# Kernel tuning notes

Hardware: AMD Instinct MI355X
Metric: run time of the kernel (lower is better)

The kernel has to match this reference:

```python
import jax, jax.numpy as jnp
import numpy as np

B, L, D, H = 2, 2048, 1024, 16
DH = D // H
EPS = 1e-5


def setup_inputs() -> dict:
    key = jax.random.key(0)
    ks = jax.random.split(key, 8)
    s = 0.02  # realistic init scale for weights
    # causal mask: True where attention is DISALLOWED (masked_fill semantics)
    mask = jnp.triu(jnp.ones((L, L), dtype=bool), k=1)[None, None]  # [1,1,L,L]
    return {
        "x": jax.random.normal(ks[0], (B, L, D), jnp.float32),
        "mask": mask,
        "ln_g": jnp.ones((D,), jnp.float32),
        "ln_b": jnp.zeros((D,), jnp.float32),
        "Wq": jax.random.normal(ks[1], (D, D), jnp.float32) * s,
        "bq": jnp.zeros((D,), jnp.float32),
        "Wk": jax.random.normal(ks[2], (D, D), jnp.float32) * s,
        "bk": jnp.zeros((D,), jnp.float32),
        "Wv": jax.random.normal(ks[3], (D, D), jnp.float32) * s,
        "bv": jnp.zeros((D,), jnp.float32),
        "Wo": jax.random.normal(ks[4], (D, D), jnp.float32) * s,
        "bo": jnp.zeros((D,), jnp.float32),
    }


def _layernorm(x, g, b):
    mu = jnp.mean(x, axis=-1, keepdims=True)
    var = jnp.var(x, axis=-1, keepdims=True)
    return (x - mu) * jax.lax.rsqrt(var + EPS) * g + b


def reference(x, mask, ln_g, ln_b, Wq, bq, Wk, bk, Wv, bv, Wo, bo):
    b, l, d = x.shape
    h = _layernorm(x, ln_g, ln_b)
    # separate Q/K/V linears, split into heads: [b, H, l, DH]
    q = (h @ Wq + bq).reshape(b, l, H, DH).transpose(0, 2, 1, 3)
    k = (h @ Wk + bk).reshape(b, l, H, DH).transpose(0, 2, 1, 3)
    v = (h @ Wv + bv).reshape(b, l, H, DH).transpose(0, 2, 1, 3)
    scale = jnp.asarray(DH, x.dtype) ** -0.5
    # full L x L score matrix (this is exactly what the torch module does)
    w = jnp.einsum("bhqd,bhkd->bhqk", q, k) * scale
    w = jnp.where(mask, -jnp.inf, w)
    w = jax.nn.softmax(w, axis=-1)
    # dropout layers are identity in eval mode
    o = jnp.einsum("bhqk,bhkd->bhqd", w, v)
    o = o.transpose(0, 2, 1, 3).reshape(b, l, d)
    return o @ Wo + bo
```

## Files before the change

### kernel.cpp

```cpp
#include <hip/hip_runtime.h>
#include <hip/hip_bf16.h>


typedef __bf16  bf16x8 __attribute__((ext_vector_type(8)));
typedef __bf16  bf16x4 __attribute__((ext_vector_type(4)));
typedef float   f32x4  __attribute__((ext_vector_type(4)));
typedef float   f32x16 __attribute__((ext_vector_type(16)));
typedef unsigned int u32x2 __attribute__((ext_vector_type(2)));
typedef unsigned int u32x4 __attribute__((ext_vector_type(4)));

#define MFMA16(a, b, c) __builtin_amdgcn_mfma_f32_16x16x32_bf16(a, b, c, 0, 0, 0)
#define MFMA32(a, b, c) __builtin_amdgcn_mfma_f32_32x32x16_bf16(a, b, c, 0, 0, 0)

#define LDT 72
#define LDO 68

#define QSCALE 0.18033688011112042f

__device__ __forceinline__ void gl_lds16(const void* g, void* l) {
    __builtin_amdgcn_global_load_lds(
        (const __attribute__((address_space(1))) void*)g,
        (__attribute__((address_space(3))) void*)l, 16, 0, 0);
}

__global__ __launch_bounds__(256) void ln_kernel(
    const float* __restrict__ x, const float* __restrict__ g,
    const float* __restrict__ bta, __hip_bfloat16* __restrict__ h)
{
    __shared__ float red[8];
    const int row = blockIdx.x, t = threadIdx.x;
    const float* xr = x + (size_t)row * 1024;
    const float4 xv = *(const float4*)(xr + t * 4);
    float s  = xv.x + xv.y + xv.z + xv.w;
    float ss = xv.x * xv.x + xv.y * xv.y + xv.z * xv.z + xv.w * xv.w;
    #pragma unroll
    for (int off = 32; off > 0; off >>= 1) {
        s  += __shfl_down(s, off);
        ss += __shfl_down(ss, off);
    }
    const int lane = t & 63, wave = t >> 6;
    if (lane == 0) { red[wave] = s; red[4 + wave] = ss; }
    __syncthreads();
    const float S  = red[0] + red[1] + red[2] + red[3];
    const float SS = red[4] + red[5] + red[6] + red[7];
    const float mu   = S * (1.0f / 1024.0f);
    const float var  = SS * (1.0f / 1024.0f) - mu * mu;
    const float rstd = rsqrtf(var + 1e-5f);
    const float4 gv = *(const float4*)(g + t * 4);
    const float4 bv = *(const float4*)(bta + t * 4);
    bf16x4 hv;
    hv[0] = (__bf16)((xv.x - mu) * rstd * gv.x + bv.x);
    hv[1] = (__bf16)((xv.y - mu) * rstd * gv.y + bv.y);
    hv[2] = (__bf16)((xv.z - mu) * rstd * gv.z + bv.z);
    hv[3] = (__bf16)((xv.w - mu) * rstd * gv.w + bv.w);
    *(bf16x4*)(h + (size_t)row * 1024 + t * 4) = hv;
}

__global__ void transpose_cast_kernel(
    const float* __restrict__ Wq, const float* __restrict__ Wk,
    const float* __restrict__ Wv, const float* __restrict__ Wo,
    __hip_bfloat16* __restrict__ tq, __hip_bfloat16* __restrict__ tk,
    __hip_bfloat16* __restrict__ tv, __hip_bfloat16* __restrict__ to_)
{
    __shared__ float t[32][33];
    const int z = blockIdx.z;
    const float* src = (z == 0) ? Wq : (z == 1) ? Wk : (z == 2) ? Wv : Wo;
    __hip_bfloat16* dst = (z == 0) ? tq : (z == 1) ? tk : (z == 2) ? tv : to_;
    const int n0 = blockIdx.x * 32, k0 = blockIdx.y * 32;
    const int tx = threadIdx.x, ty = threadIdx.y;
    t[ty][tx] = src[(size_t)(k0 + ty) * 1024 + n0 + tx];
    __syncthreads();
    dst[(size_t)(n0 + ty) * 1024 + k0 + tx] = __float2bfloat16(t[tx][ty]);
}

__device__ __forceinline__ void gemm_core_1024(
    const __hip_bfloat16* __restrict__ A, const __hip_bfloat16* __restrict__ Bt,
    int m0, int n0, f32x4 (&acc)[4][2])
{
    __shared__ __align__(16) __hip_bfloat16 sA[128 * 64];
    __shared__ __align__(16) __hip_bfloat16 sB[128 * 64];
    const int tid  = threadIdx.x;
    const int wave = tid >> 6, lane = tid & 63;
    const int quad = lane >> 4, l16 = lane & 15;
    const int wm = wave >> 2, wn = wave & 3;

    const f32x4 zero = {0.f, 0.f, 0.f, 0.f};
    #pragma unroll
    for (int i = 0; i < 4; ++i)
        #pragma unroll
        for (int j = 0; j < 2; ++j) acc[i][j] = zero;

    const int r0 = tid >> 3;
    const int c0 = (((tid & 7) ^ (r0 & 7)) << 3);
    const __hip_bfloat16* Ap = A  + (size_t)(m0 + r0) * 1024 + c0;
    const __hip_bfloat16* Bp = Bt + (size_t)(n0 + r0) * 1024 + c0;
    __hip_bfloat16* lA0 = sA + tid * 8;
    __hip_bfloat16* lB0 = sB + tid * 8;

    const int rsw = l16 & 7;

    for (int k0 = 0; k0 < 1024; k0 += 64) {
        __syncthreads();
        gl_lds16(Ap + k0, lA0);
        gl_lds16(Ap + (size_t)64 * 1024 + k0, lA0 + 64 * 64);
        gl_lds16(Bp + k0, lB0);
        gl_lds16(Bp + (size_t)64 * 1024 + k0, lB0 + 64 * 64);
        __syncthreads();
        #pragma unroll
        for (int kk = 0; kk < 64; kk += 32) {
            const int sl = (((quad + (kk >> 3)) ^ rsw) << 3);
            bf16x8 af[4], bfr[2];
            #pragma unroll
            for (int mt = 0; mt < 4; ++mt)
                af[mt] = *(const bf16x8*)(sA + (wm * 64 + mt * 16 + l16) * 64 + sl);
            #pragma unroll
            for (int nt = 0; nt < 2; ++nt)
                bfr[nt] = *(const bf16x8*)(sB + (wn * 32 + nt * 16 + l16) * 64 + sl);
            #pragma unroll
            for (int mt = 0; mt < 4; ++mt)
                #pragma unroll
                for (int nt = 0; nt < 2; ++nt)
                    acc[mt][nt] = MFMA16(af[mt], bfr[nt], acc[mt][nt]);
        }
    }
}

__global__ __launch_bounds__(512) void gemm_qkv_kernel(
    const __hip_bfloat16* __restrict__ h,
    const __hip_bfloat16* __restrict__ wt_base,
    const float* __restrict__ bq, const float* __restrict__ bk,
    const float* __restrict__ bv,
    __hip_bfloat16* __restrict__ qkv_base)
{
    const int z = blockIdx.z;
    const __hip_bfloat16* wt = wt_base + ((size_t)z << 20);
    __hip_bfloat16* outp = qkv_base + ((size_t)z << 22);

    const bool swp = (z == 2);
    const __hip_bfloat16* A  = swp ? wt : h;
    const __hip_bfloat16* Bt = swp ? h  : wt;
    const int m0 = swp ? blockIdx.x * 128 : blockIdx.y * 128;
    const int n0 = swp ? blockIdx.y * 128 : blockIdx.x * 128;

    f32x4 acc[4][2];
    gemm_core_1024(A, Bt, m0, n0, acc);

    const int lane = threadIdx.x & 63, wave = threadIdx.x >> 6;
    const int quad = lane >> 4, l16 = lane & 15;
    const int wm = wave >> 2, wn = wave & 3;

    if (!swp) {
        const float* bias = (z == 0) ? bq : bk;
        const float scale = (z == 0) ? QSCALE : 1.0f;
        #pragma unroll
        for (int mt = 0; mt < 4; ++mt)
            #pragma unroll
            for (int nt = 0; nt < 2; ++nt)
                #pragma unroll
                for (int r = 0; r < 4; ++r) {
                    const int gm = m0 + wm * 64 + mt * 16 + quad * 4 + r;
                    const int gn = n0 + wn * 32 + nt * 16 + l16;
                    const float v = (acc[mt][nt][r] + bias[gn]) * scale;
                    const int b = gm >> 11, l = gm & 2047;
                    const int hh = gn >> 6, dh = gn & 63;
                    outp[(((((size_t)(b * 16 + hh)) << 11) + l) * 64) + dh] = __float2bfloat16(v);
                }
    } else {
        #pragma unroll
        for (int mt = 0; mt < 4; ++mt)
            #pragma unroll
            for (int nt = 0; nt < 2; ++nt)
                #pragma unroll
                for (int r = 0; r < 4; ++r) {
                    const int rr = m0 + wm * 64 + mt * 16 + quad * 4 + r;
                    const int cc = n0 + wn * 32 + nt * 16 + l16;
                    const float v = acc[mt][nt][r] + bv[rr];
                    const int b = cc >> 11, l = cc & 2047;
                    const int hh = rr >> 6, dh = rr & 63;
                    outp[((((size_t)(b * 16 + hh)) * 64 + dh) << 11) + l] = __float2bfloat16(v);
                }
    }
}

__global__ __launch_bounds__(512) void gemm_out_kernel(
    const __hip_bfloat16* __restrict__ o, const __hip_bfloat16* __restrict__ wot,
    const float* __restrict__ bo, float* __restrict__ out)
{
    __shared__ __align__(16) __hip_bfloat16 sA[64 * 64];
    __shared__ __align__(16) __hip_bfloat16 sB[128 * 64];
    const int tid  = threadIdx.x;
    const int wave = tid >> 6, lane = tid & 63;
    const int quad = lane >> 4, l16 = lane & 15;
    const int wm = wave >> 2, wn = wave & 3;
    const int m0 = blockIdx.y * 64, n0 = blockIdx.x * 128;

    const f32x4 zero = {0.f, 0.f, 0.f, 0.f};
    f32x4 acc[2][2];
    #pragma unroll
    for (int i = 0; i < 2; ++i)
        #pragma unroll
        for (int j = 0; j < 2; ++j) acc[i][j] = zero;

    const int r0 = tid >> 3;
    const int c0 = (((tid & 7) ^ (r0 & 7)) << 3);
    const __hip_bfloat16* Ap = o   + (size_t)(m0 + r0) * 1024 + c0;
    const __hip_bfloat16* Bp = wot + (size_t)(n0 + r0) * 1024 + c0;
    __hip_bfloat16* lA0 = sA + tid * 8;
    __hip_bfloat16* lB0 = sB + tid * 8;

    const int rsw = l16 & 7;

    for (int k0 = 0; k0 < 1024; k0 += 64) {
        __syncthreads();
        gl_lds16(Ap + k0, lA0);
        gl_lds16(Bp + k0, lB0);
        gl_lds16(Bp + (size_t)64 * 1024 + k0, lB0 + 64 * 64);
        __syncthreads();
        #pragma unroll
        for (int kk = 0; kk < 64; kk += 32) {
            const int sl = (((quad + (kk >> 3)) ^ rsw) << 3);
            bf16x8 af[2], bfr[2];
            #pragma unroll
            for (int mt = 0; mt < 2; ++mt)
                af[mt] = *(const bf16x8*)(sA + (wm * 32 + mt * 16 + l16) * 64 + sl);
            #pragma unroll
            for (int nt = 0; nt < 2; ++nt)
                bfr[nt] = *(const bf16x8*)(sB + (wn * 32 + nt * 16 + l16) * 64 + sl);
            #pragma unroll
            for (int mt = 0; mt < 2; ++mt)
                #pragma unroll
                for (int nt = 0; nt < 2; ++nt)
                    acc[mt][nt] = MFMA16(af[mt], bfr[nt], acc[mt][nt]);
        }
    }

    #pragma unroll
    for (int mt = 0; mt < 2; ++mt)
        #pragma unroll
        for (int nt = 0; nt < 2; ++nt)
            #pragma unroll
            for (int r = 0; r < 4; ++r) {
                const int gm = m0 + wm * 32 + mt * 16 + quad * 4 + r;
                const int gn = n0 + wn * 32 + nt * 16 + l16;
                out[(size_t)gm * 1024 + gn] = acc[mt][nt][r] + bo[gn];
            }
}

__global__ __launch_bounds__(512, 4) void attn_kernel(
    const __hip_bfloat16* __restrict__ Q,
    const __hip_bfloat16* __restrict__ Kg,
    const __hip_bfloat16* __restrict__ Vt,
    __hip_bfloat16* __restrict__ O)
{
    __shared__ __align__(16) char smem[36864];
    __hip_bfloat16* sK = (__hip_bfloat16*)smem;
    __hip_bfloat16* sV = (__hip_bfloat16*)(smem + 18432);

    const int tid  = threadIdx.x;
    const int wave = tid >> 6, lane = tid & 63;
    const int grp  = wave >> 2, w4 = wave & 3;
    const int wk = w4 >> 1, wq = w4 & 1;
    const int q5 = lane & 31, hi = lane >> 5;
    const int bh = blockIdx.x;
    const int qt = 31 - blockIdx.y;
    const int q0 = qt * 64;

    const __hip_bfloat16* Qp = Q  + (size_t)bh * 2048 * 64;
    const __hip_bfloat16* Kp = Kg + (size_t)bh * 2048 * 64;
    const __hip_bfloat16* Vp = Vt + (size_t)bh * 64 * 2048;

    bf16x8 Qf[4];
    #pragma unroll
    for (int ks = 0; ks < 4; ++ks)
        Qf[ks] = *(const bf16x8*)(Qp + (size_t)(q0 + wq * 32 + q5) * 64 + ks * 16 + hi * 8);

    f32x16 o0, o1;
    #pragma unroll
    for (int r = 0; r < 16; ++r) { o0[r] = 0.f; o1[r] = 0.f; }
    float l_run = 0.f;

    const __hip_bfloat16* sKg = sK + grp * (64 * LDT);
    const __hip_bfloat16* sVg = sV + grp * (64 * LDT);
    const int qloc = wq * 32 + q5;

    const int sg = tid >> 8, tt = tid & 255;
    __hip_bfloat16* dK = sK + sg * (64 * LDT);
    __hip_bfloat16* dV = sV + sg * (64 * LDT);

    const int R = (qt + 2) >> 1;

    for (int r = 0; r < R; ++r) {
        __syncthreads();
        const int js = 2 * r + sg;
        if (js <= qt) {
            const int k0 = js * 64;
            #pragma unroll
            for (int i = 0; i < 2; ++i) {
                const int chunk = tt + 256 * i, rr = chunk >> 3, cc = (chunk & 7) << 3;
                *(int4*)(dK + rr * LDT + cc) = *(const int4*)(Kp + (size_t)(k0 + rr) * 64 + cc);
                *(int4*)(dV + rr * LDT + cc) = *(const int4*)(Vp + (size_t)rr * 2048 + k0 + cc);
            }
        }
        __syncthreads();

        const int j = 2 * r + grp;
        if (j <= qt) {
            const bool diag = (j == qt);
            f32x16 s;
            #pragma unroll
            for (int i = 0; i < 16; ++i) s[i] = 0.f;
            __builtin_amdgcn_s_setprio(1);
            #pragma unroll
            for (int ks = 0; ks < 4; ++ks) {
                const bf16x8 kf = *(const bf16x8*)(sKg + (wk * 32 + q5) * LDT + ks * 16 + hi * 8);
                s = MFMA32(kf, Qf[ks], s);
            }
            __builtin_amdgcn_s_setprio(0);
            if (diag) {
                #pragma unroll
                for (int i = 0; i < 16; ++i) {
                    const int krow = wk * 32 + (i & 3) + 8 * (i >> 2) + 4 * hi;
                    if (krow > qloc) s[i] = -1e30f;
                }
            }
            float rs = 0.f;
            u32x2 U[4];
            #pragma unroll
            for (int rb = 0; rb < 4; ++rb) {
                bf16x4 pk;
                #pragma unroll
                for (int c = 0; c < 4; ++c) {
                    const float p = exp2f(s[rb * 4 + c]);
                    rs += p;
                    pk[c] = (__bf16)p;
                }
                U[rb] = __builtin_bit_cast(u32x2, pk);
            }
            rs += __shfl_xor(rs, 32);
            l_run += rs;
            __builtin_amdgcn_s_setprio(1);
            #pragma unroll
            for (int t = 0; t < 2; ++t) {
                const unsigned p0a = __shfl_xor(U[2 * t][0], 32);
                const unsigned p0b = __shfl_xor(U[2 * t][1], 32);
                const unsigned p1a = __shfl_xor(U[2 * t + 1][0], 32);
                const unsigned p1b = __shfl_xor(U[2 * t + 1][1], 32);
                const unsigned w0 = hi ? p1a : U[2 * t][0];
                const unsigned w1 = hi ? p1b : U[2 * t][1];
                const unsigned w2 = hi ? U[2 * t + 1][0] : p0a;
                const unsigned w3 = hi ? U[2 * t + 1][1] : p0b;
                const u32x4 pw = {w0, w1, w2, w3};
                const bf16x8 pf = __builtin_bit_cast(bf16x8, pw);
                const bf16x8 vf0 = *(const bf16x8*)(sVg + (q5)      * LDT + wk * 32 + 16 * t + 8 * hi);
                const bf16x8 vf1 = *(const bf16x8*)(sVg + (32 + q5) * LDT + wk * 32 + 16 * t + 8 * hi);
                o0 = MFMA32(vf0, pf, o0);
                o1 = MFMA32(vf1, pf, o1);
            }
            __builtin_amdgcn_s_setprio(0);
        }
    }

    __syncthreads();
    float* Oscr = (float*)smem;
    float* lscr = (float*)(smem + 17408);

    if (hi == 0)
        lscr[(grp * 2 + wk) * 64 + wq * 32 + q5] = l_run;

    auto wrO = [&](bool add) {
        float* rowp = Oscr + (wq * 32 + q5) * LDO;
        #pragma unroll
        for (int d = 0; d < 2; ++d) {
            const f32x16& oc = d ? o1 : o0;
            #pragma unroll
            for (int rb = 0; rb < 4; ++rb) {
                float* p = rowp + d * 32 + 8 * rb + 4 * hi;
                f32x4 v;
                if (add) {
                    v = *(const f32x4*)p;
                    v[0] += oc[rb * 4 + 0]; v[1] += oc[rb * 4 + 1];
                    v[2] += oc[rb * 4 + 2]; v[3] += oc[rb * 4 + 3];
                } else {
                    v[0] = oc[rb * 4 + 0]; v[1] = oc[rb * 4 + 1];
                    v[2] = oc[rb * 4 + 2]; v[3] = oc[rb * 4 + 3];
                }
                *(f32x4*)p = v;
            }
        }
    };
    if (grp == 1 && wk == 1) wrO(false);
    __syncthreads();
    if (grp == 1 && wk == 0) wrO(true);
    __syncthreads();
    if (grp == 0 && wk == 1) wrO(true);
    __syncthreads();
    if (grp == 0 && wk == 0) wrO(true);
    __syncthreads();

    const int b = bh >> 4, hh = bh & 15;
    const int row = tid >> 3, col = (tid & 7) << 3;
    const float lt = lscr[(0 * 2 + 0) * 64 + row] + lscr[(0 * 2 + 1) * 64 + row]
                   + lscr[(1 * 2 + 0) * 64 + row] + lscr[(1 * 2 + 1) * 64 + row];
    const float linv = 1.0f / lt;
    const float* src = Oscr + row * LDO + col;
    const f32x4 v0 = *(const f32x4*)src;
    const f32x4 v1 = *(const f32x4*)(src + 4);
    bf16x8 ov;
    ov[0] = (__bf16)(v0[0] * linv); ov[1] = (__bf16)(v0[1] * linv);
    ov[2] = (__bf16)(v0[2] * linv); ov[3] = (__bf16)(v0[3] * linv);
    ov[4] = (__bf16)(v1[0] * linv); ov[5] = (__bf16)(v1[1] * linv);
    ov[6] = (__bf16)(v1[2] * linv); ov[7] = (__bf16)(v1[3] * linv);
    *(bf16x8*)(O + ((size_t)b * 2048 + q0 + row) * 1024 + hh * 64 + col) = ov;
}

extern "C" void kernel_launch(void* const* d_in, const int* in_sizes, int n_in,
                              void* d_out, int out_size, void* d_ws, size_t ws_size,
                              hipStream_t stream) {
    const float* x    = (const float*)d_in[0];
    const float* ln_g = (const float*)d_in[2];
    const float* ln_b = (const float*)d_in[3];
    const float* Wq = (const float*)d_in[4];  const float* bq = (const float*)d_in[5];
    const float* Wk = (const float*)d_in[6];  const float* bk = (const float*)d_in[7];
    const float* Wv = (const float*)d_in[8];  const float* bv = (const float*)d_in[9];
    const float* Wo = (const float*)d_in[10]; const float* bo = (const float*)d_in[11];
    float* out = (float*)d_out;

    __hip_bfloat16* ws = (__hip_bfloat16*)d_ws;
    const size_t M1 = 1024 * 1024;
    __hip_bfloat16* h   = ws;
    __hip_bfloat16* wqt = ws + 4 * M1;
    __hip_bfloat16* wot = ws + 7 * M1;
    __hip_bfloat16* q   = ws + 8 * M1;
    __hip_bfloat16* k   = ws + 12 * M1;
    __hip_bfloat16* vt  = ws + 16 * M1;
    __hip_bfloat16* o   = h;

    ln_kernel<<<4096, 256, 0, stream>>>(x, ln_g, ln_b, h);
    transpose_cast_kernel<<<dim3(32, 32, 4), dim3(32, 32), 0, stream>>>(
        Wq, Wk, Wv, Wo, wqt, wqt + M1, wqt + 2 * M1, wot);
    gemm_qkv_kernel<<<dim3(8, 32, 3), 512, 0, stream>>>(h, wqt, bq, bk, bv, q);
    attn_kernel<<<dim3(32, 32), 512, 0, stream>>>(q, k, vt, o);
    gemm_out_kernel<<<dim3(8, 64), 512, 0, stream>>>(o, wot, bo, out);
}
```

Before: 198.5 us.

## Double-buffer attention K/V tiles via async global_load_lds with XOR-swizzled LDS

```diff
diff --git a/kernel.cpp b/kernel.cpp
--- a/kernel.cpp
+++ b/kernel.cpp
@@ -12,7 +12,6 @@
 #define MFMA16(a, b, c) __builtin_amdgcn_mfma_f32_16x16x32_bf16(a, b, c, 0, 0, 0)
 #define MFMA32(a, b, c) __builtin_amdgcn_mfma_f32_32x32x16_bf16(a, b, c, 0, 0, 0)
 
-#define LDT 72
 #define LDO 68
 
 #define QSCALE 0.18033688011112042f
@@ -252,9 +251,9 @@
     const __hip_bfloat16* __restrict__ Vt,
     __hip_bfloat16* __restrict__ O)
 {
-    __shared__ __align__(16) char smem[36864];
+    __shared__ __align__(16) char smem[65536];
     __hip_bfloat16* sK = (__hip_bfloat16*)smem;
-    __hip_bfloat16* sV = (__hip_bfloat16*)(smem + 18432);
+    __hip_bfloat16* sV = (__hip_bfloat16*)(smem + 32768);
 
     const int tid  = threadIdx.x;
     const int wave = tid >> 6, lane = tid & 63;
@@ -279,40 +278,49 @@
     for (int r = 0; r < 16; ++r) { o0[r] = 0.f; o1[r] = 0.f; }
     float l_run = 0.f;
 
-    const __hip_bfloat16* sKg = sK + grp * (64 * LDT);
-    const __hip_bfloat16* sVg = sV + grp * (64 * LDT);
     const int qloc = wq * 32 + q5;
-
-    const int sg = tid >> 8, tt = tid & 255;
-    __hip_bfloat16* dK = sK + sg * (64 * LDT);
-    __hip_bfloat16* dV = sV + sg * (64 * LDT);
+    const int rxor = q5 & 7;
+
+    const int srow = tid >> 3;
+    const int scol = (((tid & 7) ^ (srow & 7)) << 3);
+    const __hip_bfloat16* Kst = Kp + (size_t)srow * 64 + scol;
+    const __hip_bfloat16* Vst = Vp + (size_t)srow * 2048 + scol;
+    __hip_bfloat16* dK = sK + tid * 8;
+    __hip_bfloat16* dV = sV + tid * 8;
+
+    auto stage = [&](int g, int j, int p) {
+        const int k0 = j * 64;
+        const int off = ((p * 2 + g) << 12);
+        gl_lds16(Kst + (size_t)k0 * 64, dK + off);
+        gl_lds16(Vst + k0,              dV + off);
+    };
+
+    stage(0, 0, 0);
+    if (qt >= 1) stage(1, 1, 0);
+    __syncthreads();
 
     const int R = (qt + 2) >> 1;
 
     for (int r = 0; r < R; ++r) {
-        __syncthreads();
-        const int js = 2 * r + sg;
-        if (js <= qt) {
-            const int k0 = js * 64;
-            #pragma unroll
-            for (int i = 0; i < 2; ++i) {
-                const int chunk = tt + 256 * i, rr = chunk >> 3, cc = (chunk & 7) << 3;
-                *(int4*)(dK + rr * LDT + cc) = *(const int4*)(Kp + (size_t)(k0 + rr) * 64 + cc);
-                *(int4*)(dV + rr * LDT + cc) = *(const int4*)(Vp + (size_t)rr * 2048 + k0 + cc);
-            }
+        const int p = r & 1;
+        const int jn = 2 * r + 2;
+        if (jn <= qt) {
+            stage(0, jn, p ^ 1);
+            if (jn + 1 <= qt) stage(1, jn + 1, p ^ 1);
         }
-        __syncthreads();
-
         const int j = 2 * r + grp;
         if (j <= qt) {
             const bool diag = (j == qt);
+            const __hip_bfloat16* sKg = sK + ((p * 2 + grp) << 12);
+            const __hip_bfloat16* sVg = sV + ((p * 2 + grp) << 12);
             f32x16 s;
             #pragma unroll
             for (int i = 0; i < 16; ++i) s[i] = 0.f;
             __builtin_amdgcn_s_setprio(1);
             #pragma unroll
             for (int ks = 0; ks < 4; ++ks) {
-                const bf16x8 kf = *(const bf16x8*)(sKg + (wk * 32 + q5) * LDT + ks * 16 + hi * 8);
+                const bf16x8 kf = *(const bf16x8*)(
+                    sKg + (wk * 32 + q5) * 64 + (((ks * 2 + hi) ^ rxor) << 3));
                 s = MFMA32(kf, Qf[ks], s);
             }
             __builtin_amdgcn_s_setprio(0);
@@ -330,9 +338,9 @@
                 bf16x4 pk;
                 #pragma unroll
                 for (int c = 0; c < 4; ++c) {
-                    const float p = exp2f(s[rb * 4 + c]);
-                    rs += p;
-                    pk[c] = (__bf16)p;
+                    const float p2 = exp2f(s[rb * 4 + c]);
+                    rs += p2;
+                    pk[c] = (__bf16)p2;
                 }
                 U[rb] = __builtin_bit_cast(u32x2, pk);
             }
@@ -351,16 +359,17 @@
                 const unsigned w3 = hi ? U[2 * t + 1][1] : p0b;
                 const u32x4 pw = {w0, w1, w2, w3};
                 const bf16x8 pf = __builtin_bit_cast(bf16x8, pw);
-                const bf16x8 vf0 = *(const bf16x8*)(sVg + (q5)      * LDT + wk * 32 + 16 * t + 8 * hi);
-                const bf16x8 vf1 = *(const bf16x8*)(sVg + (32 + q5) * LDT + wk * 32 + 16 * t + 8 * hi);
+                const int sl = ((wk * 4 + 2 * t + hi) ^ rxor) << 3;
+                const bf16x8 vf0 = *(const bf16x8*)(sVg + (q5)      * 64 + sl);
+                const bf16x8 vf1 = *(const bf16x8*)(sVg + (32 + q5) * 64 + sl);
                 o0 = MFMA32(vf0, pf, o0);
                 o1 = MFMA32(vf1, pf, o1);
             }
             __builtin_amdgcn_s_setprio(0);
         }
+        __syncthreads();
     }
 
-    __syncthreads();
     float* Oscr = (float*)smem;
     float* lscr = (float*)(smem + 17408);
 
```

Result: no change. 199.2 us (+0.3%).

## Shrink attention block to 4 waves with double-buffered K/V tiles

Applied to the files above, without the earlier changes.

```diff
diff --git a/kernel.cpp b/kernel.cpp
--- a/kernel.cpp
+++ b/kernel.cpp
@@ -246,7 +246,7 @@
             }
 }
 
-__global__ __launch_bounds__(512, 4) void attn_kernel(
+__global__ __launch_bounds__(256, 4) void attn_kernel(
     const __hip_bfloat16* __restrict__ Q,
     const __hip_bfloat16* __restrict__ Kg,
     const __hip_bfloat16* __restrict__ Vt,
@@ -258,8 +258,7 @@
 
     const int tid  = threadIdx.x;
     const int wave = tid >> 6, lane = tid & 63;
-    const int grp  = wave >> 2, w4 = wave & 3;
-    const int wk = w4 >> 1, wq = w4 & 1;
+    const int wk = wave >> 1, wq = wave & 1;
     const int q5 = lane & 31, hi = lane >> 5;
     const int bh = blockIdx.x;
     const int qt = 31 - blockIdx.y;
@@ -279,85 +278,81 @@
     for (int r = 0; r < 16; ++r) { o0[r] = 0.f; o1[r] = 0.f; }
     float l_run = 0.f;
 
-    const __hip_bfloat16* sKg = sK + grp * (64 * LDT);
-    const __hip_bfloat16* sVg = sV + grp * (64 * LDT);
     const int qloc = wq * 32 + q5;
 
-    const int sg = tid >> 8, tt = tid & 255;
-    __hip_bfloat16* dK = sK + sg * (64 * LDT);
-    __hip_bfloat16* dV = sV + sg * (64 * LDT);
-
-    const int R = (qt + 2) >> 1;
-
-    for (int r = 0; r < R; ++r) {
+    auto stage = [&](int j, int buf) {
+        const int k0 = j * 64;
+        __hip_bfloat16* dK = sK + buf * (64 * LDT);
+        __hip_bfloat16* dV = sV + buf * (64 * LDT);
+        #pragma unroll
+        for (int i = 0; i < 2; ++i) {
+            const int chunk = tid + 256 * i, rr = chunk >> 3, cc = (chunk & 7) << 3;
+            *(int4*)(dK + rr * LDT + cc) = *(const int4*)(Kp + (size_t)(k0 + rr) * 64 + cc);
+            *(int4*)(dV + rr * LDT + cc) = *(const int4*)(Vp + (size_t)rr * 2048 + k0 + cc);
+        }
+    };
+
+    stage(0, 0);
+
+    for (int j = 0; j <= qt; ++j) {
+        const int cur = j & 1;
         __syncthreads();
-        const int js = 2 * r + sg;
-        if (js <= qt) {
-            const int k0 = js * 64;
-            #pragma unroll
-            for (int i = 0; i < 2; ++i) {
-                const int chunk = tt + 256 * i, rr = chunk >> 3, cc = (chunk & 7) << 3;
-                *(int4*)(dK + rr * LDT + cc) = *(const int4*)(Kp + (size_t)(k0 + rr) * 64 + cc);
-                *(int4*)(dV + rr * LDT + cc) = *(const int4*)(Vp + (size_t)rr * 2048 + k0 + cc);
+        if (j < qt) stage(j + 1, cur ^ 1);
+
+        const __hip_bfloat16* sKg = sK + cur * (64 * LDT);
+        const __hip_bfloat16* sVg = sV + cur * (64 * LDT);
+        const bool diag = (j == qt);
+        f32x16 s;
+        #pragma unroll
+        for (int i = 0; i < 16; ++i) s[i] = 0.f;
+        __builtin_amdgcn_s_setprio(1);
+        #pragma unroll
+        for (int ks = 0; ks < 4; ++ks) {
+            const bf16x8 kf = *(const bf16x8*)(sKg + (wk * 32 + q5) * LDT + ks * 16 + hi * 8);
+            s = MFMA32(kf, Qf[ks], s);
+        }
+        __builtin_amdgcn_s_setprio(0);
+        if (diag) {
+            #pragma unroll
+            for (int i = 0; i < 16; ++i) {
+                const int krow = wk * 32 + (i & 3) + 8 * (i >> 2) + 4 * hi;
+                if (krow > qloc) s[i] = -1e30f;
             }
         }
-        __syncthreads();
-
-        const int j = 2 * r + grp;
-        if (j <= qt) {
-            const bool diag = (j == qt);
-            f32x16 s;
-            #pragma unroll
-            for (int i = 0; i < 16; ++i) s[i] = 0.f;
-            __builtin_amdgcn_s_setprio(1);
-            #pragma unroll
-            for (int ks = 0; ks < 4; ++ks) {
-                const bf16x8 kf = *(const bf16x8*)(sKg + (wk * 32 + q5) * LDT + ks * 16 + hi * 8);
-                s = MFMA32(kf, Qf[ks], s);
+        float rs = 0.f;
+        u32x2 U[4];
+        #pragma unroll
+        for (int rb = 0; rb < 4; ++rb) {
+            bf16x4 pk;
+            #pragma unroll
+            for (int c = 0; c < 4; ++c) {
+                const float p = exp2f(s[rb * 4 + c]);
+                rs += p;
+                pk[c] = (__bf16)p;
             }
-            __builtin_amdgcn_s_setprio(0);
-            if (diag) {
-                #pragma unroll
-                for (int i = 0; i < 16; ++i) {
-                    const int krow = wk * 32 + (i & 3) + 8 * (i >> 2) + 4 * hi;
-                    if (krow > qloc) s[i] = -1e30f;
-                }
-            }
-            float rs = 0.f;
-            u32x2 U[4];
-            #pragma unroll
-            for (int rb = 0; rb < 4; ++rb) {
-                bf16x4 pk;
-                #pragma unroll
-                for (int c = 0; c < 4; ++c) {
-                    const float p = exp2f(s[rb * 4 + c]);
-                    rs += p;
-                    pk[c] = (__bf16)p;
-                }
-                U[rb] = __builtin_bit_cast(u32x2, pk);
-            }
-            rs += __shfl_xor(rs, 32);
-            l_run += rs;
-            __builtin_amdgcn_s_setprio(1);
-            #pragma unroll
-            for (int t = 0; t < 2; ++t) {
-                const unsigned p0a = __shfl_xor(U[2 * t][0], 32);
-                const unsigned p0b = __shfl_xor(U[2 * t][1], 32);
-                const unsigned p1a = __shfl_xor(U[2 * t + 1][0], 32);
-                const unsigned p1b = __shfl_xor(U[2 * t + 1][1], 32);
-                const unsigned w0 = hi ? p1a : U[2 * t][0];
-                const unsigned w1 = hi ? p1b : U[2 * t][1];
-                const unsigned w2 = hi ? U[2 * t + 1][0] : p0a;
-                const unsigned w3 = hi ? U[2 * t + 1][1] : p0b;
-                const u32x4 pw = {w0, w1, w2, w3};
-                const bf16x8 pf = __builtin_bit_cast(bf16x8, pw);
-                const bf16x8 vf0 = *(const bf16x8*)(sVg + (q5)      * LDT + wk * 32 + 16 * t + 8 * hi);
-                const bf16x8 vf1 = *(const bf16x8*)(sVg + (32 + q5) * LDT + wk * 32 + 16 * t + 8 * hi);
-                o0 = MFMA32(vf0, pf, o0);
-                o1 = MFMA32(vf1, pf, o1);
-            }
-            __builtin_amdgcn_s_setprio(0);
-        }
+            U[rb] = __builtin_bit_cast(u32x2, pk);
+        }
+        rs += __shfl_xor(rs, 32);
+        l_run += rs;
+        __builtin_amdgcn_s_setprio(1);
+        #pragma unroll
+        for (int t = 0; t < 2; ++t) {
+            const unsigned p0a = __shfl_xor(U[2 * t][0], 32);
+            const unsigned p0b = __shfl_xor(U[2 * t][1], 32);
+            const unsigned p1a = __shfl_xor(U[2 * t + 1][0], 32);
+            const unsigned p1b = __shfl_xor(U[2 * t + 1][1], 32);
+            const unsigned w0 = hi ? p1a : U[2 * t][0];
+            const unsigned w1 = hi ? p1b : U[2 * t][1];
+            const unsigned w2 = hi ? U[2 * t + 1][0] : p0a;
+            const unsigned w3 = hi ? U[2 * t + 1][1] : p0b;
+            const u32x4 pw = {w0, w1, w2, w3};
+            const bf16x8 pf = __builtin_bit_cast(bf16x8, pw);
+            const bf16x8 vf0 = *(const bf16x8*)(sVg + (q5)      * LDT + wk * 32 + 16 * t + 8 * hi);
+            const bf16x8 vf1 = *(const bf16x8*)(sVg + (32 + q5) * LDT + wk * 32 + 16 * t + 8 * hi);
+            o0 = MFMA32(vf0, pf, o0);
+            o1 = MFMA32(vf1, pf, o1);
+        }
+        __builtin_amdgcn_s_setprio(0);
     }
 
     __syncthreads();
@@ -365,7 +360,7 @@
     float* lscr = (float*)(smem + 17408);
 
     if (hi == 0)
-        lscr[(grp * 2 + wk) * 64 + wq * 32 + q5] = l_run;
+        lscr[wk * 64 + wq * 32 + q5] = l_run;
 
     auto wrO = [&](bool add) {
         float* rowp = Oscr + (wq * 32 + q5) * LDO;
@@ -388,29 +383,28 @@
             }
         }
     };
-    if (grp == 1 && wk == 1) wrO(false);
+    if (wk == 1) wrO(false);
     __syncthreads();
-    if (grp == 1 && wk == 0) wrO(true);
+    if (wk == 0) wrO(true);
     __syncthreads();
-    if (grp == 0 && wk == 1) wrO(true);
-    __syncthreads();
-    if (grp == 0 && wk == 0) wrO(true);
-    __syncthreads();
 
     const int b = bh >> 4, hh = bh & 15;
-    const int row = tid >> 3, col = (tid & 7) << 3;
-    const float lt = lscr[(0 * 2 + 0) * 64 + row] + lscr[(0 * 2 + 1) * 64 + row]
-                   + lscr[(1 * 2 + 0) * 64 + row] + lscr[(1 * 2 + 1) * 64 + row];
-    const float linv = 1.0f / lt;
-    const float* src = Oscr + row * LDO + col;
-    const f32x4 v0 = *(const f32x4*)src;
-    const f32x4 v1 = *(const f32x4*)(src + 4);
-    bf16x8 ov;
-    ov[0] = (__bf16)(v0[0] * linv); ov[1] = (__bf16)(v0[1] * linv);
-    ov[2] = (__bf16)(v0[2] * linv); ov[3] = (__bf16)(v0[3] * linv);
-    ov[4] = (__bf16)(v1[0] * linv); ov[5] = (__bf16)(v1[1] * linv);
-    ov[6] = (__bf16)(v1[2] * linv); ov[7] = (__bf16)(v1[3] * linv);
-    *(bf16x8*)(O + ((size_t)b * 2048 + q0 + row) * 1024 + hh * 64 + col) = ov;
+    #pragma unroll
+    for (int i = 0; i < 2; ++i) {
+        const int chunk = tid + 256 * i;
+        const int row = chunk >> 3, col = (chunk & 7) << 3;
+        const float lt = lscr[0 * 64 + row] + lscr[1 * 64 + row];
+        const float linv = 1.0f / lt;
+        const float* src = Oscr + row * LDO + col;
+        const f32x4 v0 = *(const f32x4*)src;
+        const f32x4 v1 = *(const f32x4*)(src + 4);
+        bf16x8 ov;
+        ov[0] = (__bf16)(v0[0] * linv); ov[1] = (__bf16)(v0[1] * linv);
+        ov[2] = (__bf16)(v0[2] * linv); ov[3] = (__bf16)(v0[3] * linv);
+        ov[4] = (__bf16)(v1[0] * linv); ov[5] = (__bf16)(v1[1] * linv);
+        ov[6] = (__bf16)(v1[2] * linv); ov[7] = (__bf16)(v1[3] * linv);
+        *(bf16x8*)(O + ((size_t)b * 2048 + q0 + row) * 1024 + hh * 64 + col) = ov;
+    }
 }
 
 extern "C" void kernel_launch(void* const* d_in, const int* in_sizes, int n_in,
@@ -439,6 +433,6 @@
     transpose_cast_kernel<<<dim3(32, 32, 4), dim3(32, 32), 0, stream>>>(
         Wq, Wk, Wv, Wo, wqt, wqt + M1, wqt + 2 * M1, wot);
     gemm_qkv_kernel<<<dim3(8, 32, 3), 512, 0, stream>>>(h, wqt, bq, bk, bv, q);
-    attn_kernel<<<dim3(32, 32), 512, 0, stream>>>(q, k, vt, o);
+    attn_kernel<<<dim3(32, 32), 256, 0, stream>>>(q, k, vt, o);
     gemm_out_kernel<<<dim3(8, 64), 512, 0, stream>>>(o, wot, bo, out);
 }
```

Measured after the change: 200.3 us. About the same (+0.9%).
